# Kernel optimization log

Hardware: AMD Instinct MI355X
Metric: run time of the kernel (lower is better)

The kernel has to match this reference:

```python
import jax, jax.numpy as jnp
import numpy as np

N_NODES, D_NODE = 100000, 128
N_EDGES, D_EDGE = 1000000, 32
D_IN = 2 * D_NODE + D_EDGE  # 288
H1, H2, D_OUT = 128, 64, 1


def setup_inputs() -> dict:
    key = jax.random.key(0)
    ks = jax.random.split(key, 9)
    x = jax.random.normal(ks[0], (N_NODES, D_NODE), dtype=jnp.float32)
    edge_index = jax.random.randint(ks[1], (2, N_EDGES), 0, N_NODES, dtype=jnp.int64)
    edge_features = jax.random.normal(ks[2], (N_EDGES, D_EDGE), dtype=jnp.float32)
    def lin(kw, kb, fan_in, fan_out):
        bound = 1.0 / np.sqrt(fan_in)
        W = jax.random.uniform(kw, (fan_in, fan_out), minval=-bound, maxval=bound, dtype=jnp.float32)
        b = jax.random.uniform(kb, (fan_out,), minval=-bound, maxval=bound, dtype=jnp.float32)
        return W, b
    W1, b1 = lin(ks[3], ks[4], D_IN, H1)
    W2, b2 = lin(ks[5], ks[6], H1, H2)
    W3, b3 = lin(ks[7], ks[8], H2, D_OUT)
    return {"x": x, "edge_index": edge_index, "edge_features": edge_features,
            "W1": W1, "b1": b1, "W2": W2, "b2": b2, "W3": W3, "b3": b3}


def reference(x, edge_index, edge_features, W1, b1, W2, b2, W3, b3):
    origin, destination = edge_index[0], edge_index[1]
    # [E, 2*D_NODE + D_EDGE]
    z = jnp.concatenate([x[origin], x[destination], edge_features], axis=1)
    z = jax.nn.leaky_relu(z @ W1 + b1)  # negative_slope=0.01, matches torch default
    z = jax.nn.leaky_relu(z @ W2 + b2)
    z = z @ W3 + b3
    return z.reshape(-1)
```

## Files before the change

### kernel.cpp

```cpp
#include <hip/hip_runtime.h>

#define N_NODES 100000
#define N_EDGES 1000000

typedef __attribute__((ext_vector_type(8))) short bf16x8;
typedef __attribute__((ext_vector_type(4))) float f32x4;

static __device__ __forceinline__ short f2bf(float f) {
    unsigned u = __float_as_uint(f);
    u = (u + 0x7fffu + ((u >> 16) & 1u)) >> 16;
    return (short)u;
}
static __device__ __forceinline__ float bf2f(unsigned short s) {
    return __uint_as_float(((unsigned)s) << 16);
}
static __device__ __forceinline__ float lrelu(float x) {
    return fmaxf(x, 0.01f * x);
}

__global__ __launch_bounds__(256) void precompute_mfma(
    const float* __restrict__ x, const float* __restrict__ W1,
    const float* __restrict__ b1, unsigned short* __restrict__ Pb,
    unsigned short* __restrict__ Qb)
{
    const int t    = threadIdx.x;
    const int lane = t & 63;
    const int w    = t >> 6;
    const int q    = lane >> 4;
    const int n15  = lane & 15;
    const int chb  = 64 * w;

    bf16x8 afrag[4][4];
    #pragma unroll
    for (int mtl = 0; mtl < 4; ++mtl) {
        const int ch = chb + 16 * mtl + n15;
        const float* wcol = (ch < 128) ? (W1 + ch) : (W1 + 128 * 128 + (ch - 128));
        #pragma unroll
        for (int ks = 0; ks < 4; ++ks)
            #pragma unroll
            for (int j = 0; j < 8; ++j)
                afrag[mtl][ks][j] = f2bf(wcol[(size_t)(32 * ks + 8 * q + j) * 128]);
    }
    float b1r[16];
    #pragma unroll
    for (int mtl = 0; mtl < 4; ++mtl)
        #pragma unroll
        for (int r = 0; r < 4; ++r) {
            const int ch = chb + 16 * mtl + 4 * q + r;
            b1r[mtl * 4 + r] = (ch < 128) ? b1[ch] : 0.0f;
        }

    unsigned short* tbase = (w < 2) ? Pb : Qb;
    const int mtb = 4 * (w & 1);

    for (int tile = blockIdx.x; tile < N_NODES / 16; tile += gridDim.x) {
        const int n0 = tile * 16;
        const float* xrow = x + (size_t)(n0 + n15) * 128;

        bf16x8 bfr[4];
        #pragma unroll
        for (int ks = 0; ks < 4; ++ks) {
            f32x4 xa = *(const f32x4*)(xrow + 32 * ks + 8 * q);
            f32x4 xb = *(const f32x4*)(xrow + 32 * ks + 8 * q + 4);
            #pragma unroll
            for (int j = 0; j < 4; ++j) { bfr[ks][j] = f2bf(xa[j]); bfr[ks][4 + j] = f2bf(xb[j]); }
        }
        #pragma unroll
        for (int mtl = 0; mtl < 4; ++mtl) {
            f32x4 acc = {0.f, 0.f, 0.f, 0.f};
            #pragma unroll
            for (int ks = 0; ks < 4; ++ks)
                acc = __builtin_amdgcn_mfma_f32_16x16x32_bf16(afrag[mtl][ks], bfr[ks], acc, 0, 0, 0);
            unsigned short hs[4];
            #pragma unroll
            for (int r = 0; r < 4; ++r) hs[r] = (unsigned short)f2bf(acc[r] + b1r[mtl * 4 + r]);
            unsigned* dst = (unsigned*)(tbase + (size_t)(n0 + n15) * 128 + q * 32 + (mtb + mtl) * 4);
            dst[0] = (unsigned)hs[0] | ((unsigned)hs[1] << 16);
            dst[1] = (unsigned)hs[2] | ((unsigned)hs[3] << 16);
        }
    }
}

__global__ __launch_bounds__(256, 2) void edge_mfma(
    const int* __restrict__ ei, const float* __restrict__ ef,
    const float* __restrict__ W1, const float* __restrict__ W2,
    const float* __restrict__ b2, const float* __restrict__ W3,
    const float* __restrict__ b3, const unsigned short* __restrict__ Pb,
    const unsigned short* __restrict__ Qb, float* __restrict__ out)
{
    __shared__ unsigned short hbuf[4][16 * 136 + 8];
    const int t    = threadIdx.x;
    const int lane = t & 63;
    const int w    = t >> 6;
    const int q    = lane >> 4;
    const int n15  = lane & 15;
    unsigned short* hb = &hbuf[w][0];

    bf16x8 a1[8];
    #pragma unroll
    for (int mt = 0; mt < 8; ++mt)
        #pragma unroll
        for (int j = 0; j < 8; ++j)
            a1[mt][j] = f2bf(W1[(size_t)(256 + 8 * q + j) * 128 + 16 * mt + n15]);

    bf16x8 a2[4][4];
    #pragma unroll
    for (int mt2 = 0; mt2 < 4; ++mt2)
        #pragma unroll
        for (int ks = 0; ks < 4; ++ks)
            #pragma unroll
            for (int j = 0; j < 8; ++j)
                a2[mt2][ks][j] = f2bf(W2[(size_t)(32 * ks + 8 * q + j) * 64 + 16 * mt2 + n15]);

    unsigned b2w3[16];
    #pragma unroll
    for (int mt2 = 0; mt2 < 4; ++mt2)
        #pragma unroll
        for (int r = 0; r < 4; ++r) {
            const int ch = 16 * mt2 + 4 * q + r;
            b2w3[mt2 * 4 + r] = (unsigned)(unsigned short)f2bf(b2[ch])
                              | ((unsigned)(unsigned short)f2bf(W3[ch]) << 16);
        }
    const float b3v = b3[0];

    const int nTiles  = N_EDGES / 16;
    const int wid     = blockIdx.x * 4 + w;
    const int wstride = gridDim.x * 4;
    if (wid >= nTiles) return;

    int tile = wid;
    int e0   = tile * 16;
    int oi = ei[e0 + n15];
    int di = ei[N_EDGES + e0 + n15];
    f32x4 ea = *(const f32x4*)(ef + (size_t)(e0 + n15) * 32 + 8 * q);
    f32x4 eb = *(const f32x4*)(ef + (size_t)(e0 + n15) * 32 + 8 * q + 4);
    bf16x8 pvb[4], qvb[4];
    {
        const unsigned short* prow = Pb + (size_t)oi * 128 + q * 32;
        const unsigned short* qrow = Qb + (size_t)di * 128 + q * 32;
        #pragma unroll
        for (int c = 0; c < 4; ++c) {
            pvb[c] = *(const bf16x8*)(prow + 8 * c);
            qvb[c] = *(const bf16x8*)(qrow + 8 * c);
        }
    }

    while (true) {
        const int  next = tile + wstride;
        const bool have = next < nTiles;

        bf16x8 bef;
        #pragma unroll
        for (int j = 0; j < 4; ++j) { bef[j] = f2bf(ea[j]); bef[4 + j] = f2bf(eb[j]); }

        int noi = 0, ndi = 0;
        f32x4 nea = ea, neb = eb;
        if (have) {
            const int ne0 = next * 16;
            noi = ei[ne0 + n15];
            ndi = ei[N_EDGES + ne0 + n15];
            nea = *(const f32x4*)(ef + (size_t)(ne0 + n15) * 32 + 8 * q);
            neb = *(const f32x4*)(ef + (size_t)(ne0 + n15) * 32 + 8 * q + 4);
        }

        #pragma unroll
        for (int mt = 0; mt < 8; ++mt) {
            f32x4 z = {0.f, 0.f, 0.f, 0.f};
            f32x4 h = __builtin_amdgcn_mfma_f32_16x16x32_bf16(a1[mt], bef, z, 0, 0, 0);
            const int c = mt >> 1, off = (mt & 1) * 4;
            unsigned short hs[4];
            #pragma unroll
            for (int r = 0; r < 4; ++r) {
                float v = h[r] + bf2f((unsigned short)pvb[c][off + r])
                               + bf2f((unsigned short)qvb[c][off + r]);
                hs[r] = (unsigned short)f2bf(lrelu(v));
            }
            unsigned* d = (unsigned*)&hb[n15 * 136 + 16 * mt + 4 * q];
            d[0] = (unsigned)hs[0] | ((unsigned)hs[1] << 16);
            d[1] = (unsigned)hs[2] | ((unsigned)hs[3] << 16);
        }

        if (have) {
            const unsigned short* prow = Pb + (size_t)noi * 128 + q * 32;
            const unsigned short* qrow = Qb + (size_t)ndi * 128 + q * 32;
            #pragma unroll
            for (int c = 0; c < 4; ++c) {
                pvb[c] = *(const bf16x8*)(prow + 8 * c);
                qvb[c] = *(const bf16x8*)(qrow + 8 * c);
            }
        }

        __asm__ __volatile__("s_waitcnt lgkmcnt(0)" ::: "memory");

        f32x4 acc2[4] = {{0.f,0.f,0.f,0.f},{0.f,0.f,0.f,0.f},{0.f,0.f,0.f,0.f},{0.f,0.f,0.f,0.f}};
        #pragma unroll
        for (int ks = 0; ks < 4; ++ks) {
            bf16x8 hfrag = *(const bf16x8*)&hb[n15 * 136 + 32 * ks + 8 * q];
            #pragma unroll
            for (int mt2 = 0; mt2 < 4; ++mt2)
                acc2[mt2] = __builtin_amdgcn_mfma_f32_16x16x32_bf16(a2[mt2][ks], hfrag, acc2[mt2], 0, 0, 0);
        }

        float s = 0.0f;
        #pragma unroll
        for (int mt2 = 0; mt2 < 4; ++mt2)
            #pragma unroll
            for (int r = 0; r < 4; ++r) {
                const unsigned u = b2w3[mt2 * 4 + r];
                float v = acc2[mt2][r] + bf2f((unsigned short)(u & 0xffffu));
                v = lrelu(v);
                s += v * __uint_as_float(u & 0xffff0000u);
            }
        s += __shfl_xor(s, 16);
        s += __shfl_xor(s, 32);
        if (q == 0) out[e0 + n15] = s + b3v;

        if (!have) break;
        tile = next;
        e0   = next * 16;
        oi = noi; di = ndi; ea = nea; eb = neb;
    }
}

extern "C" void kernel_launch(void* const* d_in, const int* in_sizes, int n_in,
                              void* d_out, int out_size, void* d_ws, size_t ws_size,
                              hipStream_t stream) {
    const float* x   = (const float*)d_in[0];
    const int*   ei  = (const int*)d_in[1];
    const float* ef  = (const float*)d_in[2];
    const float* W1  = (const float*)d_in[3];
    const float* b1  = (const float*)d_in[4];
    const float* W2  = (const float*)d_in[5];
    const float* b2  = (const float*)d_in[6];
    const float* W3  = (const float*)d_in[7];
    const float* b3  = (const float*)d_in[8];
    float*       out = (float*)d_out;

    unsigned short* Pb = (unsigned short*)d_ws;
    unsigned short* Qb = Pb + (size_t)N_NODES * 128;

    precompute_mfma<<<2048, 256, 0, stream>>>(x, W1, b1, Pb, Qb);
    edge_mfma<<<1536, 256, 0, stream>>>(ei, ef, W1, W2, b2, W3, b3, Pb, Qb, out);
}
```

Baseline: 343.7 us.

## Move W2 fragments to LDS and stage x tiles in shared memory for occupancy

The edge kernel no longer keeps the W2 MFMA A-fragments in registers. It stages them once per block in LDS and reads them per MFMA, which frees VGPRs so launch bounds can rise to 4 blocks per CU. The precompute kernel now loads each node tile's x cooperatively, converting to bf16 in LDS, and writes 16 contiguous bf16 outputs per lane instead of scattered 4-byte stores. Grid sizes are retuned to match. The cost is extra LDS traffic and barriers in the inner loops. The early return was also removed so the new __syncthreads is safe.

New measurement: 421.6 us. +22.7%, slower.

```diff
diff --git a/kernel.cpp b/kernel.cpp
--- a/kernel.cpp
+++ b/kernel.cpp
@@ -18,11 +18,12 @@
     return fmaxf(x, 0.01f * x);
 }
 
-__global__ __launch_bounds__(256) void precompute_mfma(
+__global__ __launch_bounds__(256, 4) void precompute_mfma(
     const float* __restrict__ x, const float* __restrict__ W1,
     const float* __restrict__ b1, unsigned short* __restrict__ Pb,
     unsigned short* __restrict__ Qb)
 {
+    __shared__ unsigned short xbf[16][136];
     const int t    = threadIdx.x;
     const int lane = t & 63;
     const int w    = t >> 6;
@@ -51,43 +52,53 @@
         }
 
     unsigned short* tbase = (w < 2) ? Pb : Qb;
-    const int mtb = 4 * (w & 1);
+    const int half = (w & 1);
+
+    const int xnode = t >> 4;
+    const int xcol  = (t & 15) * 8;
 
     for (int tile = blockIdx.x; tile < N_NODES / 16; tile += gridDim.x) {
         const int n0 = tile * 16;
-        const float* xrow = x + (size_t)(n0 + n15) * 128;
-
-        bf16x8 bfr[4];
-        #pragma unroll
-        for (int ks = 0; ks < 4; ++ks) {
-            f32x4 xa = *(const f32x4*)(xrow + 32 * ks + 8 * q);
-            f32x4 xb = *(const f32x4*)(xrow + 32 * ks + 8 * q + 4);
-            #pragma unroll
-            for (int j = 0; j < 4; ++j) { bfr[ks][j] = f2bf(xa[j]); bfr[ks][4 + j] = f2bf(xb[j]); }
-        }
+
+        {
+            const float* src = x + (size_t)(n0 + xnode) * 128 + xcol;
+            f32x4 va = *(const f32x4*)src;
+            f32x4 vb = *(const f32x4*)(src + 4);
+            bf16x8 pk;
+            #pragma unroll
+            for (int j = 0; j < 4; ++j) { pk[j] = f2bf(va[j]); pk[4 + j] = f2bf(vb[j]); }
+            *(bf16x8*)&xbf[xnode][xcol] = pk;
+        }
+        __syncthreads();
+
+        unsigned short hs16[16];
         #pragma unroll
         for (int mtl = 0; mtl < 4; ++mtl) {
             f32x4 acc = {0.f, 0.f, 0.f, 0.f};
             #pragma unroll
-            for (int ks = 0; ks < 4; ++ks)
-                acc = __builtin_amdgcn_mfma_f32_16x16x32_bf16(afrag[mtl][ks], bfr[ks], acc, 0, 0, 0);
-            unsigned short hs[4];
-            #pragma unroll
-            for (int r = 0; r < 4; ++r) hs[r] = (unsigned short)f2bf(acc[r] + b1r[mtl * 4 + r]);
-            unsigned* dst = (unsigned*)(tbase + (size_t)(n0 + n15) * 128 + q * 32 + (mtb + mtl) * 4);
-            dst[0] = (unsigned)hs[0] | ((unsigned)hs[1] << 16);
-            dst[1] = (unsigned)hs[2] | ((unsigned)hs[3] << 16);
-        }
-    }
-}
-
-__global__ __launch_bounds__(256, 2) void edge_mfma(
+            for (int ks = 0; ks < 4; ++ks) {
+                bf16x8 bfr = *(const bf16x8*)&xbf[n15][32 * ks + 8 * q];
+                acc = __builtin_amdgcn_mfma_f32_16x16x32_bf16(afrag[mtl][ks], bfr, acc, 0, 0, 0);
+            }
+            #pragma unroll
+            for (int r = 0; r < 4; ++r)
+                hs16[mtl * 4 + r] = (unsigned short)f2bf(acc[r] + b1r[mtl * 4 + r]);
+        }
+        unsigned short* dst = tbase + (size_t)(n0 + n15) * 128 + q * 32 + half * 16;
+        *(bf16x8*)dst       = *(bf16x8*)&hs16[0];
+        *(bf16x8*)(dst + 8) = *(bf16x8*)&hs16[8];
+        __syncthreads();
+    }
+}
+
+__global__ __launch_bounds__(256, 4) void edge_mfma(
     const int* __restrict__ ei, const float* __restrict__ ef,
     const float* __restrict__ W1, const float* __restrict__ W2,
     const float* __restrict__ b2, const float* __restrict__ W3,
     const float* __restrict__ b3, const unsigned short* __restrict__ Pb,
     const unsigned short* __restrict__ Qb, float* __restrict__ out)
 {
+    __shared__ unsigned short w2t[16 * 64 * 8];
     __shared__ unsigned short hbuf[4][16 * 136 + 8];
     const int t    = threadIdx.x;
     const int lane = t & 63;
@@ -103,14 +114,14 @@
         for (int j = 0; j < 8; ++j)
             a1[mt][j] = f2bf(W1[(size_t)(256 + 8 * q + j) * 128 + 16 * mt + n15]);
 
-    bf16x8 a2[4][4];
-    #pragma unroll
-    for (int mt2 = 0; mt2 < 4; ++mt2)
-        #pragma unroll
-        for (int ks = 0; ks < 4; ++ks)
-            #pragma unroll
-            for (int j = 0; j < 8; ++j)
-                a2[mt2][ks][j] = f2bf(W2[(size_t)(32 * ks + 8 * q + j) * 64 + 16 * mt2 + n15]);
+    #pragma unroll
+    for (int ks = 0; ks < 4; ++ks) {
+        bf16x8 v;
+        #pragma unroll
+        for (int j = 0; j < 8; ++j)
+            v[j] = f2bf(W2[(size_t)(32 * ks + 8 * q + j) * 64 + 16 * w + n15]);
+        *(bf16x8*)&w2t[((w * 4 + ks) * 64 + lane) * 8] = v;
+    }
 
     unsigned b2w3[16];
     #pragma unroll
@@ -122,11 +133,11 @@
                               | ((unsigned)(unsigned short)f2bf(W3[ch]) << 16);
         }
     const float b3v = b3[0];
+    __syncthreads();
 
     const int nTiles  = N_EDGES / 16;
     const int wid     = blockIdx.x * 4 + w;
     const int wstride = gridDim.x * 4;
-    if (wid >= nTiles) return;
 
     int tile = wid;
     int e0   = tile * 16;
@@ -197,8 +208,10 @@
         for (int ks = 0; ks < 4; ++ks) {
             bf16x8 hfrag = *(const bf16x8*)&hb[n15 * 136 + 32 * ks + 8 * q];
             #pragma unroll
-            for (int mt2 = 0; mt2 < 4; ++mt2)
-                acc2[mt2] = __builtin_amdgcn_mfma_f32_16x16x32_bf16(a2[mt2][ks], hfrag, acc2[mt2], 0, 0, 0);
+            for (int mt2 = 0; mt2 < 4; ++mt2) {
+                bf16x8 a2f = *(const bf16x8*)&w2t[((mt2 * 4 + ks) * 64 + lane) * 8];
+                acc2[mt2] = __builtin_amdgcn_mfma_f32_16x16x32_bf16(a2f, hfrag, acc2[mt2], 0, 0, 0);
+            }
         }
 
         float s = 0.0f;
@@ -239,6 +252,6 @@
     unsigned short* Pb = (unsigned short*)d_ws;
     unsigned short* Qb = Pb + (size_t)N_NODES * 128;
 
-    precompute_mfma<<<2048, 256, 0, stream>>>(x, W1, b1, Pb, Qb);
-    edge_mfma<<<1536, 256, 0, stream>>>(ei, ef, W1, W2, b2, W3, b3, Pb, Qb, out);
-}
+    precompute_mfma<<<1024, 256, 0, stream>>>(x, W1, b1, Pb, Qb);
+    edge_mfma<<<1024, 256, 0, stream>>>(ei, ef, W1, W2, b2, W3, b3, Pb, Qb, out);
+}
```
